# Performance work log

Measured on AMD Instinct MI355X. Metric: run time of the kernel, lower is better.

The kernel has to match this reference:

```python
import jax, jax.numpy as jnp
import numpy as np

NEG_SLOPE = 0.2

def gat_conv(x, src, dst, n, W, a_src, a_dst, b):
    # PyG GATConv, heads=1: h = xW; e_ij = LeakyReLU(a_src.h_j + a_dst.h_i)
    # alpha = softmax over incoming edges of i; out_i = sum_j alpha_ij * h_j + b
    h = x @ W                               # [N, F_out]
    s_src = h @ a_src                       # [N]
    s_dst = h @ a_dst                       # [N]
    e = s_src[src] + s_dst[dst]             # [E]
    e = jnp.where(e > 0, e, NEG_SLOPE * e)  # leaky relu
    # numerically stable scatter-softmax over destination groups
    m = jax.ops.segment_max(e, dst, num_segments=n)          # [N]
    ee = jnp.exp(e - m[dst])                                  # [E]
    denom = jax.ops.segment_sum(ee, dst, num_segments=n)      # [N]
    alpha = ee / denom[dst]                                    # [E]
    out = jax.ops.segment_sum(alpha[:, None] * h[src], dst, num_segments=n)
    return out + b

def add_self_loops(edge_index, n):
    loops = jnp.arange(n, dtype=edge_index.dtype)
    src = jnp.concatenate([edge_index[0], loops])
    dst = jnp.concatenate([edge_index[1], loops])
    return src, dst

def setup_inputs() -> dict:
    key = jax.random.key(0)
    ks = jax.random.split(key, 12)
    N, E, F_IN, H1, H2, C = 50000, 800000, 1433, 512, 256, 7
    x = jax.random.normal(ks[0], (N, F_IN), dtype=jnp.float32)
    edge_index = jax.random.randint(ks[1], (2, E), 0, N, dtype=jnp.int64)
    def glorot(k, shape):
        lim = float(np.sqrt(6.0 / (shape[0] + shape[-1])))
        return jax.random.uniform(k, shape, jnp.float32, -lim, lim)
    params = {
        'W1': glorot(ks[2], (F_IN, H1)), 'as1': glorot(ks[3], (H1,)), 'ad1': glorot(ks[4], (H1,)), 'b1': jnp.zeros((H1,), jnp.float32),
        'W2': glorot(ks[5], (H1, H2)), 'as2': glorot(ks[6], (H2,)), 'ad2': glorot(ks[7], (H2,)), 'b2': jnp.zeros((H2,), jnp.float32),
        'W3': glorot(ks[8], (H2, C)), 'as3': glorot(ks[9], (C,)), 'ad3': glorot(ks[10], (C,)), 'b3': jnp.zeros((C,), jnp.float32),
    }
    return {'x': x, 'edge_index': edge_index, **params}

def reference(x, edge_index, W1, as1, ad1, b1, W2, as2, ad2, b2, W3, as3, ad3, b3):
    n = x.shape[0]
    src, dst = add_self_loops(edge_index, n)
    h = jax.nn.relu(gat_conv(x, src, dst, n, W1, as1, ad1, b1))
    h = jax.nn.relu(gat_conv(h, src, dst, n, W2, as2, ad2, b2))
    h = gat_conv(h, src, dst, n, W3, as3, ad3, b3)
    return jax.nn.log_softmax(h, axis=1)
```

## Files before the change

### kernel.cpp

```cpp
#include <hip/hip_runtime.h>
#include <hip/hip_bf16.h>
#include <math.h>

constexpr int N_NODES = 50000;
constexpr int E_EDGES = 800000;
constexpr int E_TOT   = E_EDGES + N_NODES;
constexpr int F_IN  = 1433;
constexpr int KPAD1 = 1440;
constexpr int F1 = 512;
constexpr int F2 = 256;
constexpr int NC = 7;
constexpr int MAXDEG = 1024;
constexpr float NEG_SLOPE = 0.2f;

typedef unsigned short u16;
typedef unsigned int   u32;
typedef short s16x8 __attribute__((ext_vector_type(8)));
typedef float f32x4 __attribute__((ext_vector_type(4)));

__device__ inline u16 f2b(float f) {
    u32 u = __float_as_uint(f);
    u32 r = (u + 0x7fffu + ((u >> 16) & 1u)) >> 16;
    return (u16)r;
}
__device__ inline float b2f(u16 b) { return __uint_as_float(((u32)b) << 16); }

__device__ inline u32 pkbf16(float lo, float hi) {
    union { __hip_bfloat162 h; u32 u; } c;
    c.h = __float22bfloat162_rn(make_float2(lo, hi));
    return c.u;
}

__device__ inline void gload_lds16(const void* g, void* l) {
    __builtin_amdgcn_global_load_lds(
        (const __attribute__((address_space(1))) u32*)g,
        (__attribute__((address_space(3))) u32*)l, 16, 0, 0);
}

__global__ void count_dst_kernel(const int* __restrict__ dst, int* __restrict__ counts) {
    int i = blockIdx.x * blockDim.x + threadIdx.x;
    if (i < E_TOT) {
        int d = (i < E_EDGES) ? dst[i] : (i - E_EDGES);
        atomicAdd(&counts[d], 1);
    }
}

__global__ __launch_bounds__(1024) void scan_kernel(const int* __restrict__ counts,
                                                    int* __restrict__ row_ptr, int n) {
    __shared__ int part[1024];
    int t = threadIdx.x;
    int chunk = (n + 1023) / 1024;
    int lo = t * chunk;
    int hi = min(lo + chunk, n);
    int s = 0;
    for (int i = lo; i < hi; ++i) s += counts[i];
    part[t] = s;
    __syncthreads();
    for (int off = 1; off < 1024; off <<= 1) {
        int v = 0;
        if (t >= off) v = part[t - off];
        __syncthreads();
        part[t] += v;
        __syncthreads();
    }
    int run = part[t] - s;
    for (int i = lo; i < hi; ++i) { row_ptr[i] = run; run += counts[i]; }
    if (t == 1023) row_ptr[n] = part[1023];
}

__global__ void scatter_kernel(const int* __restrict__ src, const int* __restrict__ dst,
                               const int* __restrict__ row_ptr, int* __restrict__ fill,
                               int* __restrict__ col) {
    int i = blockIdx.x * blockDim.x + threadIdx.x;
    if (i < E_TOT) {
        int s = (i < E_EDGES) ? src[i] : (i - E_EDGES);
        int d = (i < E_EDGES) ? dst[i] : (i - E_EDGES);
        int p = row_ptr[d] + atomicAdd(&fill[d], 1);
        col[p] = s;
    }
}

__global__ void convert_wt_kernel(const float* __restrict__ W, u32* __restrict__ Wt,
                                  int K, int Nn, int KP) {
    int p = blockIdx.x * blockDim.x + threadIdx.x;
    int ppr = KP / 2;
    if (p >= Nn * ppr) return;
    int n = p / ppr;
    int k = (p - n * ppr) * 2;
    float v0 = (k + 0 < K) ? W[(size_t)(k + 0) * Nn + n] : 0.f;
    float v1 = (k + 1 < K) ? W[(size_t)(k + 1) * Nn + n] : 0.f;
    Wt[p] = (u32)f2b(v0) | ((u32)f2b(v1) << 16);
}

__global__ __launch_bounds__(256, 2) void gemm1_fused(const float* __restrict__ A,
                                                      const u16* __restrict__ Bt,
                                                      u16* __restrict__ C) {
    constexpr int M = N_NODES;
    __shared__ float sA32[64 * 32];
    __shared__ u16  sAb[64 * 32];
    __shared__ u16  sB[512 * 32];
    int tid  = threadIdx.x;
    int wave = tid >> 6;
    int lane = tid & 63;
    int quad = lane >> 4;
    int lm   = lane & 15;
    int m0 = blockIdx.x * 64;

    const float* gA[2];
    float* lA[2];
#pragma unroll
    for (int c = 0; c < 2; ++c) {
        int chunk = wave * 2 + c;
        int row = min(m0 + chunk * 8 + (lane >> 3), M - 1);
        gA[c] = A + (size_t)row * F_IN + (lane & 7) * 4;
        lA[c] = &sA32[chunk * 256];
    }
    const u16* gB[8];
    u16* lB[8];
#pragma unroll
    for (int c = 0; c < 8; ++c) {
        int chunk = wave * 8 + c;
        int row = chunk * 16 + (lane >> 2);
        gB[c] = Bt + (size_t)row * KPAD1 + (lane & 3) * 8;
        lB[c] = &sB[chunk * 512];
    }

    f32x4 acc[4][8];
#pragma unroll
    for (int i = 0; i < 4; ++i)
#pragma unroll
        for (int j = 0; j < 8; ++j) acc[i][j] = (f32x4){0.f, 0.f, 0.f, 0.f};

    constexpr int K_MAIN = 1408;
    for (int k0 = 0; k0 < K_MAIN; k0 += 32) {
#pragma unroll
        for (int c = 0; c < 2; ++c) gload_lds16(gA[c] + k0, lA[c]);
#pragma unroll
        for (int c = 0; c < 8; ++c) gload_lds16(gB[c] + k0, lB[c]);
        __syncthreads();

#pragma unroll
        for (int j = 0; j < 4; ++j) {
            float2 v = *(const float2*)&sA32[2 * tid + 512 * j];
            ((u32*)sAb)[tid + 256 * j] = pkbf16(v.x, v.y);
        }
        __syncthreads();

        s16x8 af[4], bf[8];
#pragma unroll
        for (int mt = 0; mt < 4; ++mt)
            af[mt] = *(const s16x8*)&sAb[(mt * 16 + lm) * 32 + quad * 8];
#pragma unroll
        for (int nt = 0; nt < 8; ++nt)
            bf[nt] = *(const s16x8*)&sB[(wave * 128 + nt * 16 + lm) * 32 + quad * 8];
#pragma unroll
        for (int mt = 0; mt < 4; ++mt)
#pragma unroll
            for (int nt = 0; nt < 8; ++nt)
                acc[mt][nt] = __builtin_amdgcn_mfma_f32_16x16x32_bf16(
                    af[mt], bf[nt], acc[mt][nt], 0, 0, 0);
        __syncthreads();
    }

    {
        constexpr int k0 = K_MAIN;
#pragma unroll
        for (int c = 0; c < 8; ++c) gload_lds16(gB[c] + k0, lB[c]);
#pragma unroll
        for (int j = 0; j < 4; ++j) {
            int s = 2 * tid + 512 * j;
            int row = s >> 5;
            int gk = k0 + (s & 31);
            int ar = min(m0 + row, M - 1);
            const float* xr = A + (size_t)ar * F_IN;
            float v0 = (gk + 0 < F_IN) ? xr[gk + 0] : 0.f;
            float v1 = (gk + 1 < F_IN) ? xr[gk + 1] : 0.f;
            ((u32*)sAb)[tid + 256 * j] = pkbf16(v0, v1);
        }
        __syncthreads();

        s16x8 af[4], bf[8];
#pragma unroll
        for (int mt = 0; mt < 4; ++mt)
            af[mt] = *(const s16x8*)&sAb[(mt * 16 + lm) * 32 + quad * 8];
#pragma unroll
        for (int nt = 0; nt < 8; ++nt)
            bf[nt] = *(const s16x8*)&sB[(wave * 128 + nt * 16 + lm) * 32 + quad * 8];
#pragma unroll
        for (int mt = 0; mt < 4; ++mt)
#pragma unroll
            for (int nt = 0; nt < 8; ++nt)
                acc[mt][nt] = __builtin_amdgcn_mfma_f32_16x16x32_bf16(
                    af[mt], bf[nt], acc[mt][nt], 0, 0, 0);
    }

#pragma unroll
    for (int mt = 0; mt < 4; ++mt) {
        int mbase = m0 + mt * 16 + quad * 4;
#pragma unroll
        for (int nt = 0; nt < 8; ++nt) {
            int n = wave * 128 + nt * 16 + lm;
#pragma unroll
            for (int r = 0; r < 4; ++r) {
                int m = mbase + r;
                if (m < M) C[(size_t)m * F1 + n] = f2b(acc[mt][nt][r]);
            }
        }
    }
}

__global__ __launch_bounds__(256) void mfma_gemm_bt(const u16* __restrict__ A,
                                                    const u16* __restrict__ Bt,
                                                    u16* __restrict__ C,
                                                    int M, int N, int K) {
    __shared__ u16 sA[128 * 32];
    __shared__ u16 sB[128 * 32];
    int tid  = threadIdx.x;
    int wave = tid >> 6;
    int lane = tid & 63;
    int quad = lane >> 4;
    int lm   = lane & 15;
    int wm = wave & 1;
    int wn = wave >> 1;
    int m0 = blockIdx.y * 128;
    int n0 = blockIdx.x * 128;

    int ch0 = wave * 2, ch1 = wave * 2 + 1;
    int rsub = lane >> 2;
    int csub = (lane & 3) * 8;
    int ar0 = min(m0 + ch0 * 16 + rsub, M - 1);
    int ar1 = min(m0 + ch1 * 16 + rsub, M - 1);
    int br0 = n0 + ch0 * 16 + rsub;
    int br1 = n0 + ch1 * 16 + rsub;
    const u16* gA0 = A + (size_t)ar0 * K + csub;
    const u16* gA1 = A + (size_t)ar1 * K + csub;
    const u16* gB0 = Bt + (size_t)br0 * K + csub;
    const u16* gB1 = Bt + (size_t)br1 * K + csub;

    f32x4 acc[4][4];
#pragma unroll
    for (int i = 0; i < 4; ++i)
#pragma unroll
        for (int j = 0; j < 4; ++j) acc[i][j] = (f32x4){0.f, 0.f, 0.f, 0.f};

    for (int k0 = 0; k0 < K; k0 += 32) {
        gload_lds16(gA0 + k0, &sA[ch0 * 512]);
        gload_lds16(gA1 + k0, &sA[ch1 * 512]);
        gload_lds16(gB0 + k0, &sB[ch0 * 512]);
        gload_lds16(gB1 + k0, &sB[ch1 * 512]);
        __syncthreads();

        s16x8 af[4], bf[4];
#pragma unroll
        for (int mt = 0; mt < 4; ++mt)
            af[mt] = *(const s16x8*)&sA[(wm * 64 + mt * 16 + lm) * 32 + quad * 8];
#pragma unroll
        for (int nt = 0; nt < 4; ++nt)
            bf[nt] = *(const s16x8*)&sB[(wn * 64 + nt * 16 + lm) * 32 + quad * 8];
#pragma unroll
        for (int mt = 0; mt < 4; ++mt)
#pragma unroll
            for (int nt = 0; nt < 4; ++nt)
                acc[mt][nt] = __builtin_amdgcn_mfma_f32_16x16x32_bf16(
                    af[mt], bf[nt], acc[mt][nt], 0, 0, 0);
        __syncthreads();
    }

#pragma unroll
    for (int mt = 0; mt < 4; ++mt) {
        int mbase = m0 + wm * 64 + mt * 16 + quad * 4;
#pragma unroll
        for (int nt = 0; nt < 4; ++nt) {
            int n = n0 + wn * 64 + nt * 16 + lm;
#pragma unroll
            for (int r = 0; r < 4; ++r) {
                int m = mbase + r;
                if (m < M) C[(size_t)m * N + n] = f2b(acc[mt][nt][r]);
            }
        }
    }
}

template <int F>
__global__ __launch_bounds__(256) void scores_bf16_kernel(const u16* __restrict__ h,
                                                          const float* __restrict__ a_src,
                                                          const float* __restrict__ a_dst,
                                                          float* __restrict__ s_src,
                                                          float* __restrict__ s_dst, int n) {
    int gwid = (blockIdx.x * blockDim.x + threadIdx.x) >> 6;
    int lane = threadIdx.x & 63;
    if (gwid >= n) return;
    const u32* row = (const u32*)(h + (size_t)gwid * F);
    float acc1 = 0.f, acc2 = 0.f;
    for (int p = lane; p < F / 2; p += 64) {
        u32 u = row[p];
        float v0 = b2f((u16)(u & 0xffff));
        float v1 = b2f((u16)(u >> 16));
        acc1 += v0 * a_src[2 * p] + v1 * a_src[2 * p + 1];
        acc2 += v0 * a_dst[2 * p] + v1 * a_dst[2 * p + 1];
    }
#pragma unroll
    for (int o = 32; o; o >>= 1) {
        acc1 += __shfl_xor(acc1, o);
        acc2 += __shfl_xor(acc2, o);
    }
    if (lane == 0) { s_src[gwid] = acc1; s_dst[gwid] = acc2; }
}

template <int F>
__global__ __launch_bounds__(256) void scores_kernel(const float* __restrict__ h,
                                                     const float* __restrict__ a_src,
                                                     const float* __restrict__ a_dst,
                                                     float* __restrict__ s_src,
                                                     float* __restrict__ s_dst, int n) {
    int gwid = (blockIdx.x * blockDim.x + threadIdx.x) >> 6;
    int lane = threadIdx.x & 63;
    if (gwid >= n) return;
    const float* row = h + (size_t)gwid * F;
    float acc1 = 0.f, acc2 = 0.f;
    for (int f = lane; f < F; f += 64) {
        float v = row[f];
        acc1 += v * a_src[f];
        acc2 += v * a_dst[f];
    }
#pragma unroll
    for (int o = 32; o; o >>= 1) {
        acc1 += __shfl_xor(acc1, o);
        acc2 += __shfl_xor(acc2, o);
    }
    if (lane == 0) { s_src[gwid] = acc1; s_dst[gwid] = acc2; }
}

template <int F, bool OUT_BF16>
__global__ __launch_bounds__(256) void agg_gather_kernel(const u16* __restrict__ h,
                                                         const float* __restrict__ s_src,
                                                         const float* __restrict__ s_dst,
                                                         const float* __restrict__ bias,
                                                         const int* __restrict__ row_ptr,
                                                         const int* __restrict__ col,
                                                         void* __restrict__ out) {
    constexpr int UPL = F / 128;
    int node = blockIdx.x;
    int tid = threadIdx.x;
    int wave = tid >> 6;
    int lane = tid & 63;
    int beg = row_ptr[node];
    int deg = min(row_ptr[node + 1] - beg, MAXDEG);

    __shared__ float w[MAXDEG];
    __shared__ int cs[MAXDEG];
    __shared__ float sdenom;
    __shared__ float red[4][F];

    if (wave == 0) {
        float sd = s_dst[node];
        float m = -1e30f;
        for (int j = lane; j < deg; j += 64) {
            int s = col[beg + j];
            cs[j] = s;
            float e = s_src[s] + sd;
            e = (e > 0.f) ? e : NEG_SLOPE * e;
            w[j] = e;
            m = fmaxf(m, e);
        }
#pragma unroll
        for (int o = 32; o; o >>= 1) m = fmaxf(m, __shfl_xor(m, o));
        float sum = 0.f;
        for (int j = lane; j < deg; j += 64) {
            float v = expf(w[j] - m);
            w[j] = v;
            sum += v;
        }
#pragma unroll
        for (int o = 32; o; o >>= 1) sum += __shfl_xor(sum, o);
        if (lane == 0) sdenom = sum;
    }
    __syncthreads();
    float inv = 1.0f / sdenom;

    float acc[2 * UPL];
#pragma unroll
    for (int e = 0; e < 2 * UPL; ++e) acc[e] = 0.f;

    int j = wave;
    for (; j + 4 < deg; j += 8) {
        float wg0 = w[j] * inv;
        float wg1 = w[j + 4] * inv;
        const u32* r0 = (const u32*)(h + (size_t)cs[j] * F) + lane * UPL;
        const u32* r1 = (const u32*)(h + (size_t)cs[j + 4] * F) + lane * UPL;
        u32 v0[UPL], v1[UPL];
        if constexpr (UPL == 4) {
            uint4 q0 = *(const uint4*)r0; v0[0] = q0.x; v0[1] = q0.y; v0[2] = q0.z; v0[3] = q0.w;
            uint4 q1 = *(const uint4*)r1; v1[0] = q1.x; v1[1] = q1.y; v1[2] = q1.z; v1[3] = q1.w;
        } else {
            uint2 q0 = *(const uint2*)r0; v0[0] = q0.x; v0[1] = q0.y;
            uint2 q1 = *(const uint2*)r1; v1[0] = q1.x; v1[1] = q1.y;
        }
#pragma unroll
        for (int u = 0; u < UPL; ++u) {
            acc[2 * u]     += wg0 * b2f((u16)(v0[u] & 0xffff)) + wg1 * b2f((u16)(v1[u] & 0xffff));
            acc[2 * u + 1] += wg0 * b2f((u16)(v0[u] >> 16))    + wg1 * b2f((u16)(v1[u] >> 16));
        }
    }
    if (j < deg) {
        float wg = w[j] * inv;
        const u32* r = (const u32*)(h + (size_t)cs[j] * F) + lane * UPL;
        u32 v[UPL];
        if constexpr (UPL == 4) {
            uint4 q = *(const uint4*)r; v[0] = q.x; v[1] = q.y; v[2] = q.z; v[3] = q.w;
        } else {
            uint2 q = *(const uint2*)r; v[0] = q.x; v[1] = q.y;
        }
#pragma unroll
        for (int u = 0; u < UPL; ++u) {
            acc[2 * u]     += wg * b2f((u16)(v[u] & 0xffff));
            acc[2 * u + 1] += wg * b2f((u16)(v[u] >> 16));
        }
    }

#pragma unroll
    for (int e = 0; e < 2 * UPL; ++e) red[wave][lane * 2 * UPL + e] = acc[e];
    __syncthreads();

    if constexpr (OUT_BF16) {
        if (tid < F / 2) {
            int f = tid * 2;
            float v0 = red[0][f] + red[1][f] + red[2][f] + red[3][f] + bias[f];
            float v1 = red[0][f + 1] + red[1][f + 1] + red[2][f + 1] + red[3][f + 1] + bias[f + 1];
            v0 = fmaxf(v0, 0.f);
            v1 = fmaxf(v1, 0.f);
            ((u32*)out)[(size_t)node * (F / 2) + tid] = (u32)f2b(v0) | ((u32)f2b(v1) << 16);
        }
    } else {
        if (tid < F) {
            float v = red[0][tid] + red[1][tid] + red[2][tid] + red[3][tid] + bias[tid];
            ((float*)out)[(size_t)node * F + tid] = fmaxf(v, 0.f);
        }
    }
}

__global__ __launch_bounds__(64) void agg_lsm7_kernel(const float* __restrict__ h,
                                                      const float* __restrict__ s_src,
                                                      const float* __restrict__ s_dst,
                                                      const float* __restrict__ bias,
                                                      const int* __restrict__ row_ptr,
                                                      const int* __restrict__ col,
                                                      float* __restrict__ out) {
    int node = blockIdx.x;
    int lane = threadIdx.x;
    int beg = row_ptr[node];
    int deg = min(row_ptr[node + 1] - beg, MAXDEG);

    __shared__ float w[MAXDEG];
    __shared__ int cs[MAXDEG];

    float sd = s_dst[node];
    float m = -1e30f;
    for (int j = lane; j < deg; j += 64) {
        int s = col[beg + j];
        cs[j] = s;
        float e = s_src[s] + sd;
        e = (e > 0.f) ? e : NEG_SLOPE * e;
        w[j] = e;
        m = fmaxf(m, e);
    }
#pragma unroll
    for (int o = 32; o; o >>= 1) m = fmaxf(m, __shfl_xor(m, o));
    float sum = 0.f;
    for (int j = lane; j < deg; j += 64) {
        float v = expf(w[j] - m);
        w[j] = v;
        sum += v;
    }
#pragma unroll
    for (int o = 32; o; o >>= 1) sum += __shfl_xor(sum, o);
    float inv = 1.0f / sum;

    float a[NC];
#pragma unroll
    for (int f = 0; f < NC; ++f) a[f] = 0.f;
    for (int j = lane; j < deg; j += 64) {
        float wg = w[j] * inv;
        const float* row = h + (size_t)cs[j] * NC;
#pragma unroll
        for (int f = 0; f < NC; ++f) a[f] += wg * row[f];
    }
#pragma unroll
    for (int f = 0; f < NC; ++f)
#pragma unroll
        for (int o = 32; o; o >>= 1) a[f] += __shfl_xor(a[f], o);

    if (lane == 0) {
        float vals[NC];
        float mx = -1e30f;
#pragma unroll
        for (int f = 0; f < NC; ++f) { vals[f] = a[f] + bias[f]; mx = fmaxf(mx, vals[f]); }
        float ssum = 0.f;
#pragma unroll
        for (int f = 0; f < NC; ++f) ssum += expf(vals[f] - mx);
        float lse = mx + logf(ssum);
#pragma unroll
        for (int f = 0; f < NC; ++f) out[(size_t)node * NC + f] = vals[f] - lse;
    }
}

__global__ __launch_bounds__(256) void gemm3_kernel(const float* __restrict__ A,
                                                    const float* __restrict__ W,
                                                    float* __restrict__ out, int n) {
    __shared__ float sW[F2 * NC];
    for (int i = threadIdx.x; i < F2 * NC; i += blockDim.x) sW[i] = W[i];
    __syncthreads();
    int gwid = (blockIdx.x * blockDim.x + threadIdx.x) >> 6;
    int lane = threadIdx.x & 63;
    if (gwid >= n) return;
    const float* row = A + (size_t)gwid * F2;
    float4 v = *(const float4*)(row + lane * 4);
    float res = 0.f;
#pragma unroll
    for (int c = 0; c < NC; ++c) {
        float p = v.x * sW[(lane * 4 + 0) * NC + c] + v.y * sW[(lane * 4 + 1) * NC + c] +
                  v.z * sW[(lane * 4 + 2) * NC + c] + v.w * sW[(lane * 4 + 3) * NC + c];
#pragma unroll
        for (int o = 32; o; o >>= 1) p += __shfl_xor(p, o);
        if (lane == c) res = p;
    }
    if (lane < NC) out[(size_t)gwid * NC + lane] = res;
}

extern "C" void kernel_launch(void* const* d_in, const int* in_sizes, int n_in,
                              void* d_out, int out_size, void* d_ws, size_t ws_size,
                              hipStream_t stream) {
    const float* x   = (const float*)d_in[0];
    const int* ei    = (const int*)d_in[1];
    const int* src   = ei;
    const int* dst   = ei + E_EDGES;
    const float* W1  = (const float*)d_in[2];
    const float* as1 = (const float*)d_in[3];
    const float* ad1 = (const float*)d_in[4];
    const float* b1  = (const float*)d_in[5];
    const float* W2  = (const float*)d_in[6];
    const float* as2 = (const float*)d_in[7];
    const float* ad2 = (const float*)d_in[8];
    const float* b2  = (const float*)d_in[9];
    const float* W3  = (const float*)d_in[10];
    const float* as3 = (const float*)d_in[11];
    const float* ad3 = (const float*)d_in[12];
    const float* b3  = (const float*)d_in[13];
    float* outp = (float*)d_out;

    char* base = (char*)d_ws;
    u16*  a1b = (u16*)base;
    u16*  h2b = (u16*)(base + 51200000);
    float* a2 = (float*)(base + 76800000);
    float* h3 = (float*)(base + 128000000);
    u16*  h1b = (u16*)(base + 144000000);
    u16*  W1t = (u16*)(base + 195200000);
    u16*  W2t = (u16*)(base + 196674560);
    float* ssrc = (float*)(base + 196936704);
    float* sdst = (float*)(base + 197136704);
    int* row_ptr = (int*)(base + 197336704);
    int* counts  = (int*)(base + 197536708);
    int* fill    = (int*)(base + 197736708);
    int* col     = (int*)(base + 197936708);

    hipMemsetAsync(counts, 0, sizeof(int) * N_NODES, stream);
    hipMemsetAsync(fill, 0, sizeof(int) * N_NODES, stream);

    {
        int blk = 256;
        int grid = (E_TOT + blk - 1) / blk;
        count_dst_kernel<<<grid, blk, 0, stream>>>(dst, counts);
        scan_kernel<<<1, 1024, 0, stream>>>(counts, row_ptr, N_NODES);
        scatter_kernel<<<grid, blk, 0, stream>>>(src, dst, row_ptr, fill, col);
    }

    {
        int nw1 = F1 * (KPAD1 / 2);
        convert_wt_kernel<<<(nw1 + 255) / 256, 256, 0, stream>>>(W1, (u32*)W1t, F_IN, F1, KPAD1);
        int nw2 = F2 * (F1 / 2);
        convert_wt_kernel<<<(nw2 + 255) / 256, 256, 0, stream>>>(W2, (u32*)W2t, F1, F2, F1);
    }

    int waves_grid = (N_NODES + 3) / 4;
    int mblocks = (N_NODES + 127) / 128;

    {
        int grid1 = (N_NODES + 63) / 64;
        gemm1_fused<<<grid1, 256, 0, stream>>>(x, W1t, h1b);
        scores_bf16_kernel<F1><<<waves_grid, 256, 0, stream>>>(h1b, as1, ad1, ssrc, sdst, N_NODES);
        agg_gather_kernel<F1, true><<<N_NODES, 256, 0, stream>>>(
            h1b, ssrc, sdst, b1, row_ptr, col, a1b);
    }
    {
        dim3 grid(F2 / 128, mblocks);
        mfma_gemm_bt<<<grid, 256, 0, stream>>>(a1b, W2t, h2b, N_NODES, F2, F1);
        scores_bf16_kernel<F2><<<waves_grid, 256, 0, stream>>>(h2b, as2, ad2, ssrc, sdst, N_NODES);
        agg_gather_kernel<F2, false><<<N_NODES, 256, 0, stream>>>(
            h2b, ssrc, sdst, b2, row_ptr, col, a2);
    }
    {
        gemm3_kernel<<<waves_grid, 256, 0, stream>>>(a2, W3, h3, N_NODES);
        scores_kernel<NC><<<waves_grid, 256, 0, stream>>>(h3, as3, ad3, ssrc, sdst, N_NODES);
        agg_lsm7_kernel<<<N_NODES, 64, 0, stream>>>(
            h3, ssrc, sdst, b3, row_ptr, col, outp);
    }
}
```

Before: 1.094 ms.

## Double-buffer gemm1 LDS tiles with register-staged A conversion and XOR swizzle

Rewrites the first-layer GEMM main loop to double-buffer A and B tiles in LDS. The next B tile is prefetched via global_load_lds and the next A tile via vector register loads while the MFMAs run on the current buffer. A is converted to bf16 in registers and written straight to LDS, which removes the fp32 staging buffer and one barrier per iteration. An XOR swizzle on LDS slots is added to cut bank conflicts on fragment reads. LDS usage doubles for B, which may lower occupancy below the requested two blocks per CU.

Result: faster. 1.042 ms (-4.8%).

```diff
diff --git a/kernel.cpp b/kernel.cpp
--- a/kernel.cpp
+++ b/kernel.cpp
@@ -17,6 +17,7 @@
 typedef unsigned int   u32;
 typedef short s16x8 __attribute__((ext_vector_type(8)));
 typedef float f32x4 __attribute__((ext_vector_type(4)));
+typedef float float4a __attribute__((ext_vector_type(4), aligned(4)));
 
 __device__ inline u16 f2b(float f) {
     u32 u = __float_as_uint(f);
@@ -35,6 +36,18 @@
     __builtin_amdgcn_global_load_lds(
         (const __attribute__((address_space(1))) u32*)g,
         (__attribute__((address_space(3))) u32*)l, 16, 0, 0);
+}
+
+__device__ inline void loadA8(const float* p, int gk, float4a& v0, float4a& v1) {
+    if (gk + 8 <= F_IN) {
+        v0 = *(const float4a*)p;
+        v1 = *(const float4a*)(p + 4);
+    } else {
+#pragma unroll
+        for (int i = 0; i < 4; ++i) v0[i] = (gk + i < F_IN) ? p[i] : 0.f;
+#pragma unroll
+        for (int i = 0; i < 4; ++i) v1[i] = (gk + 4 + i < F_IN) ? p[4 + i] : 0.f;
+    }
 }
 
 __global__ void count_dst_kernel(const int* __restrict__ dst, int* __restrict__ counts) {
@@ -96,9 +109,10 @@
                                                       const u16* __restrict__ Bt,
                                                       u16* __restrict__ C) {
     constexpr int M = N_NODES;
-    __shared__ float sA32[64 * 32];
-    __shared__ u16  sAb[64 * 32];
-    __shared__ u16  sB[512 * 32];
+    constexpr int ABUF = 64 * 32;
+    constexpr int BBUF = 512 * 32;
+    __shared__ u16 sA[2 * ABUF];
+    __shared__ u16 sB[2 * BBUF];
     int tid  = threadIdx.x;
     int wave = tid >> 6;
     int lane = tid & 63;
@@ -106,22 +120,19 @@
     int lm   = lane & 15;
     int m0 = blockIdx.x * 64;
 
-    const float* gA[2];
-    float* lA[2];
-#pragma unroll
-    for (int c = 0; c < 2; ++c) {
-        int chunk = wave * 2 + c;
-        int row = min(m0 + chunk * 8 + (lane >> 3), M - 1);
-        gA[c] = A + (size_t)row * F_IN + (lane & 7) * 4;
-        lA[c] = &sA32[chunk * 256];
-    }
+    int arow  = min(m0 + (tid >> 2), M - 1);
+    int aslot = (tid & 3) ^ ((tid >> 3) & 3);
+    const float* xcol = A + (size_t)arow * F_IN + aslot * 8;
+    int acolbase = aslot * 8;
+
     const u16* gB[8];
     u16* lB[8];
 #pragma unroll
     for (int c = 0; c < 8; ++c) {
         int chunk = wave * 8 + c;
-        int row = chunk * 16 + (lane >> 2);
-        gB[c] = Bt + (size_t)row * KPAD1 + (lane & 3) * 8;
+        int row  = chunk * 16 + (lane >> 2);
+        int slot = (lane & 3) ^ ((lane >> 3) & 3);
+        gB[c] = Bt + (size_t)row * KPAD1 + slot * 8;
         lB[c] = &sB[chunk * 512];
     }
 
@@ -131,67 +142,57 @@
 #pragma unroll
         for (int j = 0; j < 8; ++j) acc[i][j] = (f32x4){0.f, 0.f, 0.f, 0.f};
 
-    constexpr int K_MAIN = 1408;
-    for (int k0 = 0; k0 < K_MAIN; k0 += 32) {
-#pragma unroll
-        for (int c = 0; c < 2; ++c) gload_lds16(gA[c] + k0, lA[c]);
-#pragma unroll
-        for (int c = 0; c < 8; ++c) gload_lds16(gB[c] + k0, lB[c]);
-        __syncthreads();
-
-#pragma unroll
-        for (int j = 0; j < 4; ++j) {
-            float2 v = *(const float2*)&sA32[2 * tid + 512 * j];
-            ((u32*)sAb)[tid + 256 * j] = pkbf16(v.x, v.y);
-        }
-        __syncthreads();
-
+    int rdoff = (quad ^ ((lm >> 1) & 3)) * 8;
+
+    {
+#pragma unroll
+        for (int c = 0; c < 8; ++c) gload_lds16(gB[c], lB[c]);
+        float4a a0, a1;
+        loadA8(xcol, acolbase, a0, a1);
+        uint4 pk;
+        pk.x = pkbf16(a0[0], a0[1]); pk.y = pkbf16(a0[2], a0[3]);
+        pk.z = pkbf16(a1[0], a1[1]); pk.w = pkbf16(a1[2], a1[3]);
+        *(uint4*)&sA[tid * 8] = pk;
+    }
+    __syncthreads();
+
+    int cur = 0;
+    for (int k0 = 0; k0 < KPAD1; k0 += 32) {
+        int kn = k0 + 32;
+        bool hasnext = kn < KPAD1;
+        int nxt = cur ^ 1;
+
+        float4a a0, a1;
+        if (hasnext) {
+#pragma unroll
+            for (int c = 0; c < 8; ++c) gload_lds16(gB[c] + kn, lB[c] + nxt * BBUF);
+            loadA8(xcol + kn, acolbase + kn, a0, a1);
+        }
+
+        const u16* sAc = &sA[cur * ABUF];
+        const u16* sBc = &sB[cur * BBUF];
         s16x8 af[4], bf[8];
 #pragma unroll
         for (int mt = 0; mt < 4; ++mt)
-            af[mt] = *(const s16x8*)&sAb[(mt * 16 + lm) * 32 + quad * 8];
+            af[mt] = *(const s16x8*)&sAc[(mt * 16 + lm) * 32 + rdoff];
 #pragma unroll
         for (int nt = 0; nt < 8; ++nt)
-            bf[nt] = *(const s16x8*)&sB[(wave * 128 + nt * 16 + lm) * 32 + quad * 8];
+            bf[nt] = *(const s16x8*)&sBc[(wave * 128 + nt * 16 + lm) * 32 + rdoff];
 #pragma unroll
         for (int mt = 0; mt < 4; ++mt)
 #pragma unroll
             for (int nt = 0; nt < 8; ++nt)
                 acc[mt][nt] = __builtin_amdgcn_mfma_f32_16x16x32_bf16(
                     af[mt], bf[nt], acc[mt][nt], 0, 0, 0);
+
+        if (hasnext) {
+            uint4 pk;
+            pk.x = pkbf16(a0[0], a0[1]); pk.y = pkbf16(a0[2], a0[3]);
+            pk.z = pkbf16(a1[0], a1[1]); pk.w = pkbf16(a1[2], a1[3]);
+            *(uint4*)&sA[nxt * ABUF + tid * 8] = pk;
+        }
         __syncthreads();
-    }
-
-    {
-        constexpr int k0 = K_MAIN;
-#pragma unroll
-        for (int c = 0; c < 8; ++c) gload_lds16(gB[c] + k0, lB[c]);
-#pragma unroll
-        for (int j = 0; j < 4; ++j) {
-            int s = 2 * tid + 512 * j;
-            int row = s >> 5;
-            int gk = k0 + (s & 31);
-            int ar = min(m0 + row, M - 1);
-            const float* xr = A + (size_t)ar * F_IN;
-            float v0 = (gk + 0 < F_IN) ? xr[gk + 0] : 0.f;
-            float v1 = (gk + 1 < F_IN) ? xr[gk + 1] : 0.f;
-            ((u32*)sAb)[tid + 256 * j] = pkbf16(v0, v1);
-        }
-        __syncthreads();
-
-        s16x8 af[4], bf[8];
-#pragma unroll
-        for (int mt = 0; mt < 4; ++mt)
-            af[mt] = *(const s16x8*)&sAb[(mt * 16 + lm) * 32 + quad * 8];
-#pragma unroll
-        for (int nt = 0; nt < 8; ++nt)
-            bf[nt] = *(const s16x8*)&sB[(wave * 128 + nt * 16 + lm) * 32 + quad * 8];
-#pragma unroll
-        for (int mt = 0; mt < 4; ++mt)
-#pragma unroll
-            for (int nt = 0; nt < 8; ++nt)
-                acc[mt][nt] = __builtin_amdgcn_mfma_f32_16x16x32_bf16(
-                    af[mt], bf[nt], acc[mt][nt], 0, 0, 0);
+        cur = nxt;
     }
 
 #pragma unroll
```
